# Kernel optimization log

Measured on AMD Instinct MI355X. Metric: run time of the kernel, lower is better.

## Reference

```python
import jax, jax.numpy as jnp
import numpy as np

B, N, C = 8, 512, 64
VOCAB = 200000
TEMP = 0.07
THR = 0.99
EPS = 1e-8


def _norm(x):
    # torch F.normalize: x / clamp(||x||, min=eps)
    return x / jnp.maximum(jnp.linalg.norm(x, axis=-1, keepdims=True), EPS)


def setup_inputs() -> dict:
    key = jax.random.key(0)
    k = jax.random.split(key, 6)
    return {
        "Q": jax.random.normal(k[0], (B, N, C), dtype=jnp.float32),
        "Pos": jax.random.normal(k[1], (B, N, C), dtype=jnp.float32),
        "neg_global": jax.random.normal(k[2], (B, N, C), dtype=jnp.float32),
        "pos_item_ids": jax.random.randint(k[3], (B, N), 0, VOCAB),
        "neg_global_item_ids": jax.random.randint(k[4], (B, N), 0, VOCAB),
        "log_q_table": jax.random.normal(k[5], (VOCAB,), dtype=jnp.float32),
    }


def reference(Q, Pos, neg_global, pos_item_ids, neg_global_item_ids, log_q_table):
    B_, N_, C_ = Q.shape
    BN = B_ * N_
    Qn, Pn, Gn = _norm(Q), _norm(Pos), _norm(neg_global)
    Qf = Qn.reshape(BN, C_)
    Pf = Pn.reshape(BN, C_)
    Nf = Gn.reshape(BN, C_)
    pos_ids = pos_item_ids.reshape(BN)
    neg_ids = neg_global_item_ids.reshape(BN)
    row_seq = jnp.arange(BN) // N_  # sequence index of each flattened row
    neg_inf = jnp.float32(-jnp.inf)

    # ---- global negatives ----
    p2n = (Pf @ Nf.T).reshape(B_, N_, BN)            # (B, N, BN) cosine Pos vs neg
    ok_glob = (jnp.max(p2n, axis=1) <= THR)[row_seq]  # (BN, BN) per-seq max mask
    sim_glob = (Qf @ Nf.T) / TEMP
    logits_glob = jnp.where(ok_glob, sim_glob - log_q_table[neg_ids][None, :], neg_inf)

    # ---- in-batch negatives ----
    p2p = (Pf @ Pf.T).reshape(B_, N_, BN)
    diff_seq = row_seq[:, None] != row_seq[None, :]
    ok_ibn = (jnp.max(p2p, axis=1) <= THR)[row_seq] & diff_seq
    sim_ibn = (Qf @ Pf.T) / TEMP
    logits_ibn = jnp.where(ok_ibn, sim_ibn - log_q_table[pos_ids][None, :], neg_inf)

    # ---- positive logits ----
    pos_logits = (jnp.sum(Qn * Pn, axis=-1) / TEMP).reshape(BN, 1)
    pos_logits = pos_logits - log_q_table[pos_ids][:, None]

    # concat: (BN, 1 + 2*BN)
    return jnp.concatenate([pos_logits, logits_glob, logits_ibn], axis=1)
```

## Files before the change

kernel.cpp:

```cpp
#include <hip/hip_runtime.h>
#include <math.h>

#define B_  8
#define N_  512
#define C_  64
#define BN  4096
#define OUTW 8193
#define INV_TEMP 14.285714285714286f
#define THR_ 0.99f
#define NEG_HUGE -1e30f

typedef __attribute__((ext_vector_type(8))) short short8v;
typedef __attribute__((ext_vector_type(4))) float f32x4;

#define WSB_QN   0
#define WSB_PN   (512*1024)
#define WSB_GN   (1024*1024)
#define WSB_LQP  (1536*1024)
#define WSB_LQN  (WSB_LQP + 16*1024)
#define WSB_MAXG (WSB_LQP + 32*1024)
#define WSB_MAXI (WSB_MAXG + 128*1024)

__device__ __forceinline__ unsigned short f2bf(float f) {
  unsigned u = __float_as_uint(f);
  u += 0x7fffu + ((u >> 16) & 1u);
  return (unsigned short)(u >> 16);
}

__device__ __forceinline__ void load_lds16(const void* g, void* l) {
  __builtin_amdgcn_global_load_lds(
      (const __attribute__((address_space(1))) unsigned int*)g,
      (__attribute__((address_space(3))) unsigned int*)l, 16, 0, 0);
}

__global__ __launch_bounds__(256) void kprep(const float* __restrict__ Q,
    const float* __restrict__ P, const float* __restrict__ G,
    const int* __restrict__ pos_ids, const int* __restrict__ neg_ids,
    const float* __restrict__ table, unsigned short* __restrict__ wbf,
    float* __restrict__ lqp, float* __restrict__ lqn, float* __restrict__ out) {
  int gw   = blockIdx.x * 4 + (threadIdx.x >> 6);
  int lane = threadIdx.x & 63;
  int t = gw >> 12, r = gw & 4095;
  const float* src = (t == 0) ? Q : (t == 1 ? P : G);
  float x = src[(size_t)r * C_ + lane];
  float s = x * x;
  #pragma unroll
  for (int off = 32; off; off >>= 1) s += __shfl_xor(s, off);
  float inv = 1.0f / fmaxf(sqrtf(s), 1e-8f);
  wbf[(size_t)t * BN * C_ + (size_t)r * C_ + lane] = f2bf(x * inv);

  if (t == 0) {
    float p = P[(size_t)r * C_ + lane];
    float pp = p * p, qp = x * p;
    #pragma unroll
    for (int off = 32; off; off >>= 1) {
      pp += __shfl_xor(pp, off);
      qp += __shfl_xor(qp, off);
    }
    if (lane == 0) {
      float d = qp / (fmaxf(sqrtf(s), 1e-8f) * fmaxf(sqrtf(pp), 1e-8f));
      float lp = table[pos_ids[r]];
      out[(size_t)r * OUTW] = d * INV_TEMP - lp;
      lqp[r] = lp;
      lqn[r] = table[neg_ids[r]];
    }
  }
}

__global__ __launch_bounds__(256) void kmaskM(const unsigned short* __restrict__ PN,
    const unsigned short* __restrict__ GN, float* __restrict__ maxout) {
  __shared__ uint4 A4[1024];
  __shared__ uint4 B4[1024];
  __shared__ float red[2][128];
  int tid = threadIdx.x;
  int jt = blockIdx.x, b = blockIdx.y, z = blockIdx.z;
  const unsigned short* X = z ? PN : GN;
  int j0 = jt * 128;

  #pragma unroll
  for (int it = 0; it < 4; ++it) {
    int idx = tid + 256 * it, row = idx >> 3, kc = idx & 7;
    load_lds16(X + (size_t)(j0 + row) * C_ + (kc ^ (row & 7)) * 8, &B4[idx]);
  }
  int wid = tid >> 6, lane = tid & 63;
  int m0 = (wid >> 1) * 64, n0 = (wid & 1) * 64;
  int lr = lane & 15, lk = lane >> 4;
  const short8v* As = (const short8v*)A4;
  const short8v* Bs = (const short8v*)B4;
  float mcol[4] = {NEG_HUGE, NEG_HUGE, NEG_HUGE, NEG_HUGE};

  for (int ch = 0; ch < 4; ++ch) {
    __syncthreads();
    #pragma unroll
    for (int it = 0; it < 4; ++it) {
      int idx = tid + 256 * it, row = idx >> 3, kc = idx & 7;
      load_lds16(PN + (size_t)(b * N_ + ch * 128 + row) * C_ + (kc ^ (row & 7)) * 8,
                 &A4[idx]);
    }
    __syncthreads();

    f32x4 zz = {0.f, 0.f, 0.f, 0.f};
    f32x4 acc[4][4];
    #pragma unroll
    for (int mf = 0; mf < 4; ++mf)
      #pragma unroll
      for (int nf = 0; nf < 4; ++nf) acc[mf][nf] = zz;

    #pragma unroll
    for (int ks = 0; ks < 2; ++ks) {
      int kc = lk + ks * 4;
      short8v a[4], bgs[4];
      #pragma unroll
      for (int mf = 0; mf < 4; ++mf) {
        int r = m0 + mf * 16 + lr;
        a[mf] = As[r * 8 + (kc ^ (r & 7))];
      }
      #pragma unroll
      for (int nf = 0; nf < 4; ++nf) {
        int r = n0 + nf * 16 + lr;
        bgs[nf] = Bs[r * 8 + (kc ^ (r & 7))];
      }
      #pragma unroll
      for (int mf = 0; mf < 4; ++mf)
        #pragma unroll
        for (int nf = 0; nf < 4; ++nf)
          acc[mf][nf] = __builtin_amdgcn_mfma_f32_16x16x32_bf16(
              a[mf], bgs[nf], acc[mf][nf], 0, 0, 0);
    }
    #pragma unroll
    for (int nf = 0; nf < 4; ++nf)
      #pragma unroll
      for (int mf = 0; mf < 4; ++mf)
        #pragma unroll
        for (int rg = 0; rg < 4; ++rg)
          mcol[nf] = fmaxf(mcol[nf], acc[mf][nf][rg]);
  }
  #pragma unroll
  for (int nf = 0; nf < 4; ++nf) {
    float v = mcol[nf];
    v = fmaxf(v, __shfl_xor(v, 16));
    v = fmaxf(v, __shfl_xor(v, 32));
    mcol[nf] = v;
  }
  int wn = wid >> 1, wj = wid & 1;
  if (lane < 16) {
    #pragma unroll
    for (int nf = 0; nf < 4; ++nf)
      red[wn][wj * 64 + nf * 16 + lane] = mcol[nf];
  }
  __syncthreads();
  if (tid < 128)
    maxout[(size_t)(z * 8 + b) * 4096 + j0 + tid] =
        fmaxf(red[0][tid], red[1][tid]);
}

__global__ __launch_bounds__(256) void klogitsM(const unsigned short* __restrict__ QN,
    const unsigned short* __restrict__ PN, const unsigned short* __restrict__ GN,
    const float* __restrict__ lqp, const float* __restrict__ lqn,
    const float* __restrict__ maxg, const float* __restrict__ maxi,
    float* __restrict__ out) {
  __shared__ uint4 AB4[2048];
  __shared__ float oks[128];
  __shared__ float lqs[128];
  int tid = threadIdx.x;
  int jt = blockIdx.x, half = jt >> 5;
  int j0 = (jt & 31) * 128;
  int i0 = blockIdx.y * 128;
  size_t colbase = 1 + (size_t)half * BN + j0;

  if (half && ((i0 >> 9) == (j0 >> 9))) {
    float4 nh = {NEG_HUGE, NEG_HUGE, NEG_HUGE, NEG_HUGE};
    #pragma unroll
    for (int it = 0; it < 16; ++it) {
      int idx = tid + 256 * it;
      int row = idx >> 5, c4 = (idx & 31) * 4;
      *(float4*)(out + (size_t)(i0 + row) * OUTW + colbase + c4) = nh;
    }
    return;
  }

  const unsigned short* X = half ? PN : GN;
  const float* lq = half ? lqp : lqn;
  const float* mc = (half ? maxi : maxg) + (size_t)(i0 >> 9) * 4096;

  if (tid < 128) {
    oks[tid] = (mc[j0 + tid] <= THR_) ? 1.0f : 0.0f;
    lqs[tid] = lq[j0 + tid];
  }
  #pragma unroll
  for (int it = 0; it < 4; ++it) {
    int idx = tid + 256 * it, row = idx >> 3, kc = idx & 7;
    int sc = (kc ^ (row & 7)) * 8;
    load_lds16(QN + (size_t)(i0 + row) * C_ + sc, &AB4[idx]);
    load_lds16(X  + (size_t)(j0 + row) * C_ + sc, &AB4[1024 + idx]);
  }
  __syncthreads();

  int wid = tid >> 6, lane = tid & 63;
  int m0 = (wid >> 1) * 64, n0 = (wid & 1) * 64;
  int lr = lane & 15, lk = lane >> 4;
  const short8v* As = (const short8v*)AB4;
  const short8v* Bs = (const short8v*)(AB4 + 1024);

  f32x4 zz = {0.f, 0.f, 0.f, 0.f};
  f32x4 acc[4][4];
  #pragma unroll
  for (int mf = 0; mf < 4; ++mf)
    #pragma unroll
    for (int nf = 0; nf < 4; ++nf) acc[mf][nf] = zz;

  #pragma unroll
  for (int ks = 0; ks < 2; ++ks) {
    int kc = lk + ks * 4;
    short8v a[4], bgs[4];
    #pragma unroll
    for (int mf = 0; mf < 4; ++mf) {
      int r = m0 + mf * 16 + lr;
      a[mf] = As[r * 8 + (kc ^ (r & 7))];
    }
    #pragma unroll
    for (int nf = 0; nf < 4; ++nf) {
      int r = n0 + nf * 16 + lr;
      bgs[nf] = Bs[r * 8 + (kc ^ (r & 7))];
    }
    #pragma unroll
    for (int mf = 0; mf < 4; ++mf)
      #pragma unroll
      for (int nf = 0; nf < 4; ++nf)
        acc[mf][nf] = __builtin_amdgcn_mfma_f32_16x16x32_bf16(
            a[mf], bgs[nf], acc[mf][nf], 0, 0, 0);
  }

  float* stage = (float*)AB4;
  int wm = wid >> 1;
  #pragma unroll
  for (int h = 0; h < 2; ++h) {
    __syncthreads();
    if (wm == h) {
      #pragma unroll
      for (int nf = 0; nf < 4; ++nf) {
        int j = n0 + nf * 16 + lr;
        float okv = oks[j];
        float lqv = lqs[j];
        #pragma unroll
        for (int mf = 0; mf < 4; ++mf) {
          #pragma unroll
          for (int rg = 0; rg < 4; ++rg) {
            int row = mf * 16 + lk * 4 + rg;
            float v = acc[mf][nf][rg] * INV_TEMP - lqv;
            v = (okv != 0.0f) ? v : NEG_HUGE;
            int cq = (j >> 2) ^ ((row >> 2) & 7);
            stage[row * 128 + cq * 4 + (j & 3)] = v;
          }
        }
      }
    }
    __syncthreads();
    #pragma unroll
    for (int it = 0; it < 8; ++it) {
      int idx = tid + 256 * it;
      int row = idx >> 5, q = idx & 31;
      int cq = q ^ ((row >> 2) & 7);
      float4 v = *(const float4*)(stage + row * 128 + cq * 4);
      *(float4*)(out + (size_t)(i0 + h * 64 + row) * OUTW + colbase + q * 4) = v;
    }
  }
}

extern "C" void kernel_launch(void* const* d_in, const int* in_sizes, int n_in,
                              void* d_out, int out_size, void* d_ws, size_t ws_size,
                              hipStream_t stream) {
  const float* Q = (const float*)d_in[0];
  const float* P = (const float*)d_in[1];
  const float* G = (const float*)d_in[2];
  const int* pos_ids = (const int*)d_in[3];
  const int* neg_ids = (const int*)d_in[4];
  const float* table = (const float*)d_in[5];
  float* out = (float*)d_out;
  char* w = (char*)d_ws;
  unsigned short* QN = (unsigned short*)(w + WSB_QN);
  unsigned short* PN = (unsigned short*)(w + WSB_PN);
  unsigned short* GN = (unsigned short*)(w + WSB_GN);
  float* LQP = (float*)(w + WSB_LQP);
  float* LQN = (float*)(w + WSB_LQN);
  float* MAXG = (float*)(w + WSB_MAXG);
  float* MAXI = (float*)(w + WSB_MAXI);

  kprep<<<dim3(3 * BN / 4), 256, 0, stream>>>(Q, P, G, pos_ids, neg_ids, table,
                                              QN, LQP, LQN, out);
  kmaskM<<<dim3(32, 8, 2), 256, 0, stream>>>(PN, GN, MAXG);
  klogitsM<<<dim3(64, 32), 256, 0, stream>>>(QN, PN, GN, LQP, LQN,
                                             MAXG, MAXI, out);
}
```

Before: 168.2 us.

## Double-buffer mask-kernel LDS loads, rebalance logits warp tiling, use nontemporal output stores

The mask kernel now double-buffers the Pos chunk tiles in LDS, prefetching the next chunk while the current one is computed, and drops one barrier per iteration. The logits kernel reassigns its MFMA tiles so every wave owns 16-row stripes in both halves with all 128 columns. This lets all four waves write staging in each half instead of only two waves idling through the other half. Output stores become nontemporal to avoid polluting cache with the large write-only logits matrix. The cost is more LDS in the mask kernel and possible reliance on async LDS-load ordering across the single barrier.

```diff
diff --git a/kernel.cpp b/kernel.cpp
--- a/kernel.cpp
+++ b/kernel.cpp
@@ -69,8 +69,8 @@
 
 __global__ __launch_bounds__(256) void kmaskM(const unsigned short* __restrict__ PN,
     const unsigned short* __restrict__ GN, float* __restrict__ maxout) {
-  __shared__ uint4 A4[1024];
   __shared__ uint4 B4[1024];
+  __shared__ uint4 A4[2][1024];
   __shared__ float red[2][128];
   int tid = threadIdx.x;
   int jt = blockIdx.x, b = blockIdx.y, z = blockIdx.z;
@@ -81,23 +81,27 @@
   for (int it = 0; it < 4; ++it) {
     int idx = tid + 256 * it, row = idx >> 3, kc = idx & 7;
     load_lds16(X + (size_t)(j0 + row) * C_ + (kc ^ (row & 7)) * 8, &B4[idx]);
+    load_lds16(PN + (size_t)(b * N_ + row) * C_ + (kc ^ (row & 7)) * 8,
+               &A4[0][idx]);
   }
   int wid = tid >> 6, lane = tid & 63;
   int m0 = (wid >> 1) * 64, n0 = (wid & 1) * 64;
   int lr = lane & 15, lk = lane >> 4;
-  const short8v* As = (const short8v*)A4;
   const short8v* Bs = (const short8v*)B4;
   float mcol[4] = {NEG_HUGE, NEG_HUGE, NEG_HUGE, NEG_HUGE};
 
   for (int ch = 0; ch < 4; ++ch) {
     __syncthreads();
-    #pragma unroll
-    for (int it = 0; it < 4; ++it) {
-      int idx = tid + 256 * it, row = idx >> 3, kc = idx & 7;
-      load_lds16(PN + (size_t)(b * N_ + ch * 128 + row) * C_ + (kc ^ (row & 7)) * 8,
-                 &A4[idx]);
-    }
-    __syncthreads();
+    if (ch < 3) {
+      #pragma unroll
+      for (int it = 0; it < 4; ++it) {
+        int idx = tid + 256 * it, row = idx >> 3, kc = idx & 7;
+        load_lds16(PN + (size_t)(b * N_ + (ch + 1) * 128 + row) * C_ +
+                       (kc ^ (row & 7)) * 8,
+                   &A4[(ch + 1) & 1][idx]);
+      }
+    }
+    const short8v* As = (const short8v*)A4[ch & 1];
 
     f32x4 zz = {0.f, 0.f, 0.f, 0.f};
     f32x4 acc[4][4];
@@ -169,12 +173,13 @@
   size_t colbase = 1 + (size_t)half * BN + j0;
 
   if (half && ((i0 >> 9) == (j0 >> 9))) {
-    float4 nh = {NEG_HUGE, NEG_HUGE, NEG_HUGE, NEG_HUGE};
+    f32x4 nh = {NEG_HUGE, NEG_HUGE, NEG_HUGE, NEG_HUGE};
     #pragma unroll
     for (int it = 0; it < 16; ++it) {
       int idx = tid + 256 * it;
       int row = idx >> 5, c4 = (idx & 31) * 4;
-      *(float4*)(out + (size_t)(i0 + row) * OUTW + colbase + c4) = nh;
+      __builtin_nontemporal_store(nh,
+          (f32x4*)(out + (size_t)(i0 + row) * OUTW + colbase + c4));
     }
     return;
   }
@@ -197,62 +202,55 @@
   __syncthreads();
 
   int wid = tid >> 6, lane = tid & 63;
-  int m0 = (wid >> 1) * 64, n0 = (wid & 1) * 64;
   int lr = lane & 15, lk = lane >> 4;
   const short8v* As = (const short8v*)AB4;
   const short8v* Bs = (const short8v*)(AB4 + 1024);
 
   f32x4 zz = {0.f, 0.f, 0.f, 0.f};
-  f32x4 acc[4][4];
-  #pragma unroll
-  for (int mf = 0; mf < 4; ++mf)
-    #pragma unroll
-    for (int nf = 0; nf < 4; ++nf) acc[mf][nf] = zz;
+  f32x4 acc[2][8];
+  #pragma unroll
+  for (int mh = 0; mh < 2; ++mh)
+    #pragma unroll
+    for (int nf = 0; nf < 8; ++nf) acc[mh][nf] = zz;
 
   #pragma unroll
   for (int ks = 0; ks < 2; ++ks) {
     int kc = lk + ks * 4;
-    short8v a[4], bgs[4];
-    #pragma unroll
-    for (int mf = 0; mf < 4; ++mf) {
-      int r = m0 + mf * 16 + lr;
-      a[mf] = As[r * 8 + (kc ^ (r & 7))];
-    }
-    #pragma unroll
-    for (int nf = 0; nf < 4; ++nf) {
-      int r = n0 + nf * 16 + lr;
-      bgs[nf] = Bs[r * 8 + (kc ^ (r & 7))];
-    }
-    #pragma unroll
-    for (int mf = 0; mf < 4; ++mf)
-      #pragma unroll
-      for (int nf = 0; nf < 4; ++nf)
-        acc[mf][nf] = __builtin_amdgcn_mfma_f32_16x16x32_bf16(
-            a[mf], bgs[nf], acc[mf][nf], 0, 0, 0);
+    short8v a2[2], bb[8];
+    #pragma unroll
+    for (int mh = 0; mh < 2; ++mh) {
+      int r = mh * 64 + wid * 16 + lr;
+      a2[mh] = As[r * 8 + (kc ^ (r & 7))];
+    }
+    #pragma unroll
+    for (int nf = 0; nf < 8; ++nf) {
+      int r = nf * 16 + lr;
+      bb[nf] = Bs[r * 8 + (kc ^ (r & 7))];
+    }
+    #pragma unroll
+    for (int mh = 0; mh < 2; ++mh)
+      #pragma unroll
+      for (int nf = 0; nf < 8; ++nf)
+        acc[mh][nf] = __builtin_amdgcn_mfma_f32_16x16x32_bf16(
+            a2[mh], bb[nf], acc[mh][nf], 0, 0, 0);
   }
 
   float* stage = (float*)AB4;
-  int wm = wid >> 1;
   #pragma unroll
   for (int h = 0; h < 2; ++h) {
     __syncthreads();
-    if (wm == h) {
-      #pragma unroll
-      for (int nf = 0; nf < 4; ++nf) {
-        int j = n0 + nf * 16 + lr;
-        float okv = oks[j];
-        float lqv = lqs[j];
-        #pragma unroll
-        for (int mf = 0; mf < 4; ++mf) {
-          #pragma unroll
-          for (int rg = 0; rg < 4; ++rg) {
-            int row = mf * 16 + lk * 4 + rg;
-            float v = acc[mf][nf][rg] * INV_TEMP - lqv;
-            v = (okv != 0.0f) ? v : NEG_HUGE;
-            int cq = (j >> 2) ^ ((row >> 2) & 7);
-            stage[row * 128 + cq * 4 + (j & 3)] = v;
-          }
-        }
+    #pragma unroll
+    for (int nf = 0; nf < 8; ++nf) {
+      int j = nf * 16 + lr;
+      float okv = oks[j];
+      float lqv = lqs[j];
+      #pragma unroll
+      for (int rg = 0; rg < 4; ++rg) {
+        int rowh = wid * 16 + lk * 4 + rg;
+        float v = acc[h][nf][rg] * INV_TEMP - lqv;
+        v = (okv != 0.0f) ? v : NEG_HUGE;
+        int cq = (j >> 2) ^ ((rowh >> 2) & 7);
+        stage[rowh * 128 + cq * 4 + (j & 3)] = v;
       }
     }
     __syncthreads();
@@ -261,8 +259,9 @@
       int idx = tid + 256 * it;
       int row = idx >> 5, q = idx & 31;
       int cq = q ^ ((row >> 2) & 7);
-      float4 v = *(const float4*)(stage + row * 128 + cq * 4);
-      *(float4*)(out + (size_t)(i0 + h * 64 + row) * OUTW + colbase + q * 4) = v;
+      f32x4 v = *(const f32x4*)(stage + row * 128 + cq * 4);
+      __builtin_nontemporal_store(v,
+          (f32x4*)(out + (size_t)(i0 + h * 64 + row) * OUTW + colbase + q * 4));
     }
   }
 }
```

Result: slower. 180.9 us (+7.6%).
